# Performance work log

Hardware: AMD Instinct MI355X
Metric: run time of the kernel (lower is better)

The kernel has to match this reference:

```python
import jax, jax.numpy as jnp
import numpy as np

H = 256       # hidden_dim
E = H // 2    # operator embedding dim
T = 12        # num_tempers
O = 3         # num_ops per temper
HOPS = 4      # max_path_hops
B = 128       # batch
D = 2048      # input_dim
NCLS = 10     # task_head classes


def setup_inputs() -> dict:
    key = jax.random.key(0)
    ks = jax.random.split(key, 12)
    x = jax.random.normal(ks[0], (B, D), jnp.float32)
    N = B * (D // H)  # 1024 patch tokens
    # per-hop routed temper per patch; value == T means halt
    sampled_tempers = jax.random.randint(ks[1], (HOPS, N), 0, T + 1, jnp.int32)
    sampled_ops = jax.random.randint(ks[2], (HOPS, N), 0, O, jnp.int32)
    s1 = 1.0 / np.sqrt(H + E)
    W1 = jax.random.uniform(ks[3], (T, O, H + E, H), jnp.float32, -s1, s1)
    b1 = jax.random.uniform(ks[4], (T, O, H), jnp.float32, -s1, s1)
    s2 = 1.0 / np.sqrt(H)
    W2 = jax.random.uniform(ks[5], (T, O, H, H), jnp.float32, -s2, s2)
    b2 = jax.random.uniform(ks[6], (T, O, H), jnp.float32, -s2, s2)
    op_emb = jax.random.normal(ks[7], (T, O, E), jnp.float32)
    ln_g = jnp.ones((H,), jnp.float32)
    ln_b = jnp.zeros((H,), jnp.float32)
    Wt = jax.random.uniform(ks[8], (H, NCLS), jnp.float32, -s2, s2)
    bt = jax.random.uniform(ks[9], (NCLS,), jnp.float32, -s2, s2)
    return dict(x=x, W1=W1, b1=b1, W2=W2, b2=b2, op_emb=op_emb,
                ln_g=ln_g, ln_b=ln_b, Wt=Wt, bt=bt,
                sampled_tempers=sampled_tempers, sampled_ops=sampled_ops)


def reference(x, W1, b1, W2, b2, op_emb, ln_g, ln_b, Wt, bt,
              sampled_tempers, sampled_ops):
    Bsz, Din = x.shape
    pad = (-Din) % H
    if pad > 0:
        x = jnp.pad(x, ((0, 0), (0, pad)))
    state = x.reshape(-1, H)                       # [N, H] patch states
    active = jnp.ones((state.shape[0],), bool)     # not-yet-halted mask
    for hop in range(HOPS):
        t = sampled_tempers[hop]
        o = sampled_ops[hop]
        active = active & (t != T)                 # T == halt action
        tc = jnp.clip(t, 0, T - 1)                 # safe index for halted rows
        emb = op_emb[tc, o]                        # [N, E] op embedding gather
        xa = jnp.concatenate([state, emb], axis=-1)  # [N, H+E]
        # per-token expert weight gather + batched matvec (memory-bound dispatch)
        h = jax.nn.relu(jnp.einsum('ni,nio->no', xa, W1[tc, o]) + b1[tc, o])
        y = jax.nn.relu(jnp.einsum('ni,nio->no', h, W2[tc, o]) + b2[tc, o])
        state = jnp.where(active[:, None], y, state)
    pooled = state.reshape(Bsz, -1, H).mean(axis=1)   # [B, H]
    mu = pooled.mean(axis=-1, keepdims=True)
    var = pooled.var(axis=-1, keepdims=True)
    normed = (pooled - mu) * jax.lax.rsqrt(var + 1e-5) * ln_g + ln_b
    return normed @ Wt + bt                           # [B, 10]
```

## Files before the change

kernel.cpp:

```cpp
#include <hip/hip_runtime.h>

typedef __attribute__((ext_vector_type(8))) short short8;
typedef __attribute__((ext_vector_type(4))) float floatx4;

#define NEXP   36
#define NTOK   1024
#define HOPS   4

#define OFF_STATE   0u
#define OFF_W1B     1048576u
#define OFF_W2B     5767168u
#define OFF_C1      10485760u
#define OFF_COUNTS  10522624u
#define OFF_LISTS   10523264u

__device__ __forceinline__ unsigned short f2bf(float f) {
    unsigned u = __float_as_uint(f);
    u += 0x7FFFu + ((u >> 16) & 1u);
    return (unsigned short)(u >> 16);
}

__global__ __launch_bounds__(256) void prep_kernel(
    const float* __restrict__ x, const float* __restrict__ W1,
    const float* __restrict__ b1, const float* __restrict__ W2,
    const float* __restrict__ op_emb,
    const int* __restrict__ tempers, const int* __restrict__ ops,
    float* __restrict__ state, unsigned short* __restrict__ W1b,
    unsigned short* __restrict__ W2b, float* __restrict__ c1,
    int* __restrict__ counts, int* __restrict__ lists)
{
    const int bid = blockIdx.x;
    const int t = threadIdx.x;

    if (bid < 2304) {
        const int mat = bid / 1152;
        const int id  = bid % 1152;
        const int e   = id / 32;
        const int sub = id % 32;
        const int kb  = sub / 4;
        const int jt  = sub % 4;
        const float* src = mat ? (W2 + e * 65536) : (W1 + e * 98304);
        unsigned short* dst = (mat ? W2b : W1b) + e * 65536;
        const int j  = jt * 64 + (t & 63);
        const int ks = (t >> 6) * 8;
        short8 v;
        #pragma unroll
        for (int i = 0; i < 8; i++)
            v[i] = (short)f2bf(src[(kb * 32 + ks + i) * 256 + j]);
        *(short8*)(dst + (kb * 256 + j) * 32 + ks) = v;
    } else if (bid < 2340) {
        const int e = bid - 2304;
        __shared__ float eb[128];
        if (t < 128) eb[t] = op_emb[e * 128 + t];
        __syncthreads();
        float acc = b1[e * 256 + t];
        const float* wp = W1 + e * 98304 + 256 * 256;
        #pragma unroll 4
        for (int k = 0; k < 128; k++)
            acc += eb[k] * wp[k * 256 + t];
        c1[e * 256 + t] = acc;
    } else if (bid < 2404) {
        const int cb = bid - 2340;
        const float4* xs = (const float4*)x;
        float4* ss = (float4*)state;
        #pragma unroll
        for (int p = 0; p < 4; p++) {
            int i4 = cb * 1024 + p * 256 + t;
            ss[i4] = xs[i4];
        }
    } else {
        __shared__ int lc[HOPS * NEXP];
        if (t < HOPS * NEXP) lc[t] = 0;
        __syncthreads();
        for (int q = 0; q < 4; q++) {
            int n = q * 256 + t;
            bool act = true;
            for (int hop = 0; hop < HOPS; hop++) {
                int tt = tempers[hop * NTOK + n];
                int oo = ops[hop * NTOK + n];
                act = act && (tt != 12);
                if (act) {
                    int e = tt * 3 + oo;
                    int pos = atomicAdd(&lc[hop * NEXP + e], 1);
                    lists[(hop * NEXP + e) * NTOK + pos] = n;
                }
            }
        }
        __syncthreads();
        if (t < HOPS * NEXP) counts[t] = lc[t];
    }
}

__global__ __launch_bounds__(256) void hop_kernel(
    float* __restrict__ state,
    const unsigned short* __restrict__ W1b,
    const unsigned short* __restrict__ W2b,
    const float* __restrict__ c1, const float* __restrict__ b2,
    const int* __restrict__ counts, const int* __restrict__ lists, int hop)
{
    const int e    = blockIdx.x % NEXP;
    const int tile = blockIdx.x / NEXP;
    const int n_e  = counts[hop * NEXP + e];
    const int m0   = tile * 16;
    if (m0 >= n_e) return;
    const int mact = min(16, n_e - m0);

    __shared__ int toks[16];
    __shared__ unsigned short Ab[4096];
    __shared__ unsigned short Hb[4096];

    const int t = threadIdx.x;
    if (t < 16) toks[t] = (t < mact) ? lists[(hop * NEXP + e) * NTOK + m0 + t] : 0;
    __syncthreads();

    #pragma unroll
    for (int p = 0; p < 4; p++) {
        int idx = p * 256 + t;
        int m = idx >> 6;
        int c4 = idx & 63;
        int k = c4 * 4;
        float4 v = make_float4(0.f, 0.f, 0.f, 0.f);
        if (m < mact) v = *(const float4*)(state + toks[m] * 256 + k);
        int kb = k >> 5, g = (k >> 3) & 3, i = k & 7;
        unsigned short* d = Ab + kb * 512 + (g * 16 + m) * 8 + i;
        d[0] = f2bf(v.x); d[1] = f2bf(v.y); d[2] = f2bf(v.z); d[3] = f2bf(v.w);
    }
    __syncthreads();

    const int l = t & 63, w = t >> 6;
    const int col = l & 15, g = l >> 4;

    floatx4 acc[4];
    #pragma unroll
    for (int jt = 0; jt < 4; jt++) {
        float cv = c1[e * 256 + w * 64 + jt * 16 + col];
        acc[jt] = (floatx4){cv, cv, cv, cv};
    }
    const unsigned short* Wp = W1b + e * 65536;
    #pragma unroll
    for (int kb = 0; kb < 8; kb++) {
        short8 a = *(const short8*)(Ab + kb * 512 + l * 8);
        #pragma unroll
        for (int jt = 0; jt < 4; jt++) {
            int j = w * 64 + jt * 16 + col;
            short8 bfrg = *(const short8*)(Wp + (kb * 256 + j) * 32 + g * 8);
            acc[jt] = __builtin_amdgcn_mfma_f32_16x16x32_bf16(a, bfrg, acc[jt], 0, 0, 0);
        }
    }
    #pragma unroll
    for (int jt = 0; jt < 4; jt++) {
        int kh = w * 64 + jt * 16 + col;
        int kb2 = kh >> 5, g2 = (kh >> 3) & 3, i2 = kh & 7;
        #pragma unroll
        for (int r = 0; r < 4; r++) {
            int m = g * 4 + r;
            float vv = acc[jt][r];
            vv = vv > 0.f ? vv : 0.f;
            Hb[kb2 * 512 + (g2 * 16 + m) * 8 + i2] = f2bf(vv);
        }
    }
    __syncthreads();

    #pragma unroll
    for (int jt = 0; jt < 4; jt++) {
        float bv = b2[e * 256 + w * 64 + jt * 16 + col];
        acc[jt] = (floatx4){bv, bv, bv, bv};
    }
    const unsigned short* Wp2 = W2b + e * 65536;
    #pragma unroll
    for (int kb = 0; kb < 8; kb++) {
        short8 a = *(const short8*)(Hb + kb * 512 + l * 8);
        #pragma unroll
        for (int jt = 0; jt < 4; jt++) {
            int j = w * 64 + jt * 16 + col;
            short8 bfrg = *(const short8*)(Wp2 + (kb * 256 + j) * 32 + g * 8);
            acc[jt] = __builtin_amdgcn_mfma_f32_16x16x32_bf16(a, bfrg, acc[jt], 0, 0, 0);
        }
    }
    #pragma unroll
    for (int jt = 0; jt < 4; jt++) {
        int j = w * 64 + jt * 16 + col;
        #pragma unroll
        for (int r = 0; r < 4; r++) {
            int m = g * 4 + r;
            if (m < mact) {
                float vv = acc[jt][r];
                state[toks[m] * 256 + j] = vv > 0.f ? vv : 0.f;
            }
        }
    }
}

__global__ __launch_bounds__(256) void final_kernel(
    const float* __restrict__ state, const float* __restrict__ ln_g,
    const float* __restrict__ ln_b, const float* __restrict__ Wt,
    const float* __restrict__ bt, float* __restrict__ out)
{
    const int b = blockIdx.x, t = threadIdx.x;
    float s = 0.f;
    #pragma unroll
    for (int p = 0; p < 8; p++) s += state[(b * 8 + p) * 256 + t];
    s *= 0.125f;

    float v1 = s, v2 = s * s;
    #pragma unroll
    for (int off = 32; off; off >>= 1) {
        v1 += __shfl_down(v1, off);
        v2 += __shfl_down(v2, off);
    }
    __shared__ float red[8];
    __shared__ float stats[2];
    const int w = t >> 6, l = t & 63;
    if (l == 0) { red[w] = v1; red[4 + w] = v2; }
    __syncthreads();
    if (t == 0) {
        float su = red[0] + red[1] + red[2] + red[3];
        float sq = red[4] + red[5] + red[6] + red[7];
        float mu = su * (1.0f / 256.0f);
        float var = sq * (1.0f / 256.0f) - mu * mu;
        stats[0] = mu;
        stats[1] = rsqrtf(var + 1e-5f);
    }
    __syncthreads();
    float normed = (s - stats[0]) * stats[1] * ln_g[t] + ln_b[t];

    __shared__ float pr[40];
    #pragma unroll
    for (int c = 0; c < 10; c++) {
        float pv = normed * Wt[t * 10 + c];
        #pragma unroll
        for (int off = 32; off; off >>= 1) pv += __shfl_down(pv, off);
        if (l == 0) pr[w * 10 + c] = pv;
    }
    __syncthreads();
    if (t < 10)
        out[b * 10 + t] = pr[t] + pr[10 + t] + pr[20 + t] + pr[30 + t] + bt[t];
}

extern "C" void kernel_launch(void* const* d_in, const int* in_sizes, int n_in,
                              void* d_out, int out_size, void* d_ws, size_t ws_size,
                              hipStream_t stream)
{
    const float* x      = (const float*)d_in[0];
    const float* W1     = (const float*)d_in[1];
    const float* b1     = (const float*)d_in[2];
    const float* W2     = (const float*)d_in[3];
    const float* b2     = (const float*)d_in[4];
    const float* op_emb = (const float*)d_in[5];
    const float* ln_g   = (const float*)d_in[6];
    const float* ln_b   = (const float*)d_in[7];
    const float* Wt     = (const float*)d_in[8];
    const float* bt     = (const float*)d_in[9];
    const int* tempers  = (const int*)d_in[10];
    const int* ops      = (const int*)d_in[11];

    char* ws = (char*)d_ws;
    float* state          = (float*)(ws + OFF_STATE);
    unsigned short* W1b   = (unsigned short*)(ws + OFF_W1B);
    unsigned short* W2b   = (unsigned short*)(ws + OFF_W2B);
    float* c1             = (float*)(ws + OFF_C1);
    int* counts           = (int*)(ws + OFF_COUNTS);
    int* lists            = (int*)(ws + OFF_LISTS);
    float* out            = (float*)d_out;

    prep_kernel<<<2405, 256, 0, stream>>>(x, W1, b1, W2, op_emb, tempers, ops,
                                          state, W1b, W2b, c1, counts, lists);
    for (int hop = 0; hop < HOPS; hop++)
        hop_kernel<<<2304, 256, 0, stream>>>(state, W1b, W2b, c1, b2,
                                             counts, lists, hop);
    final_kernel<<<128, 256, 0, stream>>>(state, ln_g, ln_b, Wt, bt, out);
}
```

Measured before the change: 152.2 us.

## Fuse hop and final kernels into persistent kernel with grid barriers and job lists

Replaces the four per-hop kernel launches and the final kernel with a single persistent kernel of 256 blocks. It walks a compact job list built in prep, where each job is one (expert, 16-token tile), and separates hops with an atomic-counter grid barrier. The aim is to cut launch overhead and the mostly-empty blocks of the 2304-block grid. The barrier assumes all 256 blocks are co-resident, and it adds spin-wait cost and fewer parallel blocks per hop.

```diff
diff --git a/kernel.cpp b/kernel.cpp
--- a/kernel.cpp
+++ b/kernel.cpp
@@ -6,6 +6,7 @@
 #define NEXP   36
 #define NTOK   1024
 #define HOPS   4
+#define PGRID  256
 
 #define OFF_STATE   0u
 #define OFF_W1B     1048576u
@@ -13,6 +14,9 @@
 #define OFF_C1      10485760u
 #define OFF_COUNTS  10522624u
 #define OFF_LISTS   10523264u
+#define OFF_JOBS    11113088u
+#define OFF_NJ      11115136u
+#define OFF_BAR     11115152u
 
 __device__ __forceinline__ unsigned short f2bf(float f) {
     unsigned u = __float_as_uint(f);
@@ -27,7 +31,8 @@
     const int* __restrict__ tempers, const int* __restrict__ ops,
     float* __restrict__ state, unsigned short* __restrict__ W1b,
     unsigned short* __restrict__ W2b, float* __restrict__ c1,
-    int* __restrict__ counts, int* __restrict__ lists)
+    int* __restrict__ counts, int* __restrict__ lists,
+    int* __restrict__ jobs, int* __restrict__ njobs, int* __restrict__ bar)
 {
     const int bid = blockIdx.x;
     const int t = threadIdx.x;
@@ -71,6 +76,7 @@
     } else {
         __shared__ int lc[HOPS * NEXP];
         if (t < HOPS * NEXP) lc[t] = 0;
+        if (t == 0) bar[0] = 0;
         __syncthreads();
         for (int q = 0; q < 4; q++) {
             int n = q * 256 + t;
@@ -88,28 +94,45 @@
         }
         __syncthreads();
         if (t < HOPS * NEXP) counts[t] = lc[t];
-    }
-}
-
-__global__ __launch_bounds__(256) void hop_kernel(
-    float* __restrict__ state,
+        if (t < HOPS) {
+            int hop = t, nj = 0;
+            for (int e = 0; e < NEXP; e++) {
+                int c = lc[hop * NEXP + e];
+                for (int m0 = 0; m0 < c; m0 += 16)
+                    jobs[hop * 128 + nj++] = (m0 << 8) | e;
+            }
+            njobs[hop] = nj;
+        }
+    }
+}
+
+__device__ __forceinline__ void grid_barrier(int* bar, int target) {
+    __syncthreads();
+    if (threadIdx.x == 0) {
+        __threadfence();
+        __hip_atomic_fetch_add(bar, 1, __ATOMIC_RELEASE, __HIP_MEMORY_SCOPE_AGENT);
+        while (__hip_atomic_load(bar, __ATOMIC_ACQUIRE, __HIP_MEMORY_SCOPE_AGENT) < target)
+            __builtin_amdgcn_s_sleep(2);
+        __threadfence();
+    }
+    __syncthreads();
+}
+
+__device__ __forceinline__ void do_job(
+    int hop, int job, float* __restrict__ state,
     const unsigned short* __restrict__ W1b,
     const unsigned short* __restrict__ W2b,
     const float* __restrict__ c1, const float* __restrict__ b2,
-    const int* __restrict__ counts, const int* __restrict__ lists, int hop)
+    const int* __restrict__ counts, const int* __restrict__ lists,
+    int* toks, unsigned short* Ab, unsigned short* Hb)
 {
-    const int e    = blockIdx.x % NEXP;
-    const int tile = blockIdx.x / NEXP;
-    const int n_e  = counts[hop * NEXP + e];
-    const int m0   = tile * 16;
-    if (m0 >= n_e) return;
+    const int e   = job & 0xFF;
+    const int m0  = job >> 8;
+    const int n_e = counts[hop * NEXP + e];
     const int mact = min(16, n_e - m0);
-
-    __shared__ int toks[16];
-    __shared__ unsigned short Ab[4096];
-    __shared__ unsigned short Hb[4096];
-
     const int t = threadIdx.x;
+
+    __syncthreads();
     if (t < 16) toks[t] = (t < mact) ? lists[(hop * NEXP + e) * NTOK + m0 + t] : 0;
     __syncthreads();
 
@@ -191,12 +214,33 @@
     }
 }
 
-__global__ __launch_bounds__(256) void final_kernel(
-    const float* __restrict__ state, const float* __restrict__ ln_g,
-    const float* __restrict__ ln_b, const float* __restrict__ Wt,
-    const float* __restrict__ bt, float* __restrict__ out)
+__global__ __launch_bounds__(256) void persist_kernel(
+    float* __restrict__ state,
+    const unsigned short* __restrict__ W1b,
+    const unsigned short* __restrict__ W2b,
+    const float* __restrict__ c1, const float* __restrict__ b2,
+    const int* __restrict__ counts, const int* __restrict__ lists,
+    const int* __restrict__ jobs, const int* __restrict__ njobs,
+    int* __restrict__ bar,
+    const float* __restrict__ ln_g, const float* __restrict__ ln_b,
+    const float* __restrict__ Wt, const float* __restrict__ bt,
+    float* __restrict__ out)
 {
-    const int b = blockIdx.x, t = threadIdx.x;
+    __shared__ int toks[16];
+    __shared__ unsigned short Ab[4096];
+    __shared__ unsigned short Hb[4096];
+
+    for (int hop = 0; hop < HOPS; hop++) {
+        const int nj = njobs[hop];
+        for (int j = blockIdx.x; j < nj; j += PGRID)
+            do_job(hop, jobs[hop * 128 + j], state, W1b, W2b, c1, b2,
+                   counts, lists, toks, Ab, Hb);
+        grid_barrier(bar, (hop + 1) * PGRID);
+    }
+
+    const int b = blockIdx.x;
+    if (b >= 128) return;
+    const int t = threadIdx.x;
     float s = 0.f;
     #pragma unroll
     for (int p = 0; p < 8; p++) s += state[(b * 8 + p) * 256 + t];
@@ -261,12 +305,15 @@
     float* c1             = (float*)(ws + OFF_C1);
     int* counts           = (int*)(ws + OFF_COUNTS);
     int* lists            = (int*)(ws + OFF_LISTS);
+    int* jobs             = (int*)(ws + OFF_JOBS);
+    int* njobs            = (int*)(ws + OFF_NJ);
+    int* bar              = (int*)(ws + OFF_BAR);
     float* out            = (float*)d_out;
 
     prep_kernel<<<2405, 256, 0, stream>>>(x, W1, b1, W2, op_emb, tempers, ops,
-                                          state, W1b, W2b, c1, counts, lists);
-    for (int hop = 0; hop < HOPS; hop++)
-        hop_kernel<<<2304, 256, 0, stream>>>(state, W1b, W2b, c1, b2,
-                                             counts, lists, hop);
-    final_kernel<<<128, 256, 0, stream>>>(state, ln_g, ln_b, Wt, bt, out);
-}
+                                          state, W1b, W2b, c1, counts, lists,
+                                          jobs, njobs, bar);
+    persist_kernel<<<PGRID, 256, 0, stream>>>(state, W1b, W2b, c1, b2,
+                                              counts, lists, jobs, njobs, bar,
+                                              ln_g, ln_b, Wt, bt, out);
+}
```

Measured after the change: 319.2 us. 110% more time.

## Build compact per-hop job list and use 1024-thread blocks per expert tile

Applied to the files above, without the earlier changes.

The prep kernel now builds a dense list of (expert, tile) jobs per hop, so the hop kernel launches only 128 blocks that index into that list. Before, it launched 2304 blocks, most of which exited immediately. Each block now uses 16 waves, one per 16-column slice, instead of 4 waves each covering 64 columns. This cuts empty-block launch overhead and spreads the weight loads over more waves. In exchange, each wave has less independent MFMA work to hide latency, and the job list is built serially by 4 threads, which adds work to prep.

```diff
diff --git a/kernel.cpp b/kernel.cpp
--- a/kernel.cpp
+++ b/kernel.cpp
@@ -13,6 +13,8 @@
 #define OFF_C1      10485760u
 #define OFF_COUNTS  10522624u
 #define OFF_LISTS   10523264u
+#define OFF_JOBS    11113088u
+#define OFF_NJ      11115136u
 
 __device__ __forceinline__ unsigned short f2bf(float f) {
     unsigned u = __float_as_uint(f);
@@ -27,7 +29,8 @@
     const int* __restrict__ tempers, const int* __restrict__ ops,
     float* __restrict__ state, unsigned short* __restrict__ W1b,
     unsigned short* __restrict__ W2b, float* __restrict__ c1,
-    int* __restrict__ counts, int* __restrict__ lists)
+    int* __restrict__ counts, int* __restrict__ lists,
+    int* __restrict__ jobs, int* __restrict__ njobs)
 {
     const int bid = blockIdx.x;
     const int t = threadIdx.x;
@@ -88,21 +91,31 @@
         }
         __syncthreads();
         if (t < HOPS * NEXP) counts[t] = lc[t];
-    }
-}
-
-__global__ __launch_bounds__(256) void hop_kernel(
+        if (t < HOPS) {
+            int hop = t, nj = 0;
+            for (int e = 0; e < NEXP; e++) {
+                int c = lc[hop * NEXP + e];
+                for (int m0 = 0; m0 < c; m0 += 16)
+                    jobs[hop * 128 + nj++] = (m0 << 8) | e;
+            }
+            njobs[hop] = nj;
+        }
+    }
+}
+
+__global__ __launch_bounds__(1024) void hop_kernel(
     float* __restrict__ state,
     const unsigned short* __restrict__ W1b,
     const unsigned short* __restrict__ W2b,
     const float* __restrict__ c1, const float* __restrict__ b2,
-    const int* __restrict__ counts, const int* __restrict__ lists, int hop)
-{
-    const int e    = blockIdx.x % NEXP;
-    const int tile = blockIdx.x / NEXP;
-    const int n_e  = counts[hop * NEXP + e];
-    const int m0   = tile * 16;
-    if (m0 >= n_e) return;
+    const int* __restrict__ counts, const int* __restrict__ lists,
+    const int* __restrict__ jobs, const int* __restrict__ njobs, int hop)
+{
+    if (blockIdx.x >= njobs[hop]) return;
+    const int job = jobs[hop * 128 + blockIdx.x];
+    const int e   = job & 0xFF;
+    const int m0  = job >> 8;
+    const int n_e = counts[hop * NEXP + e];
     const int mact = min(16, n_e - m0);
 
     __shared__ int toks[16];
@@ -113,12 +126,9 @@
     if (t < 16) toks[t] = (t < mact) ? lists[(hop * NEXP + e) * NTOK + m0 + t] : 0;
     __syncthreads();
 
-    #pragma unroll
-    for (int p = 0; p < 4; p++) {
-        int idx = p * 256 + t;
-        int m = idx >> 6;
-        int c4 = idx & 63;
-        int k = c4 * 4;
+    {
+        int m = t >> 6;
+        int k = (t & 63) * 4;
         float4 v = make_float4(0.f, 0.f, 0.f, 0.f);
         if (m < mact) v = *(const float4*)(state + toks[m] * 256 + k);
         int kb = k >> 5, g = (k >> 3) & 3, i = k & 7;
@@ -129,64 +139,50 @@
 
     const int l = t & 63, w = t >> 6;
     const int col = l & 15, g = l >> 4;
-
-    floatx4 acc[4];
-    #pragma unroll
-    for (int jt = 0; jt < 4; jt++) {
-        float cv = c1[e * 256 + w * 64 + jt * 16 + col];
-        acc[jt] = (floatx4){cv, cv, cv, cv};
+    const int j = w * 16 + col;
+
+    floatx4 acc;
+    {
+        float cv = c1[e * 256 + j];
+        acc = (floatx4){cv, cv, cv, cv};
     }
     const unsigned short* Wp = W1b + e * 65536;
     #pragma unroll
     for (int kb = 0; kb < 8; kb++) {
         short8 a = *(const short8*)(Ab + kb * 512 + l * 8);
-        #pragma unroll
-        for (int jt = 0; jt < 4; jt++) {
-            int j = w * 64 + jt * 16 + col;
-            short8 bfrg = *(const short8*)(Wp + (kb * 256 + j) * 32 + g * 8);
-            acc[jt] = __builtin_amdgcn_mfma_f32_16x16x32_bf16(a, bfrg, acc[jt], 0, 0, 0);
-        }
-    }
-    #pragma unroll
-    for (int jt = 0; jt < 4; jt++) {
-        int kh = w * 64 + jt * 16 + col;
+        short8 bfrg = *(const short8*)(Wp + (kb * 256 + j) * 32 + g * 8);
+        acc = __builtin_amdgcn_mfma_f32_16x16x32_bf16(a, bfrg, acc, 0, 0, 0);
+    }
+    {
+        int kh = j;
         int kb2 = kh >> 5, g2 = (kh >> 3) & 3, i2 = kh & 7;
         #pragma unroll
         for (int r = 0; r < 4; r++) {
             int m = g * 4 + r;
-            float vv = acc[jt][r];
+            float vv = acc[r];
             vv = vv > 0.f ? vv : 0.f;
             Hb[kb2 * 512 + (g2 * 16 + m) * 8 + i2] = f2bf(vv);
         }
     }
     __syncthreads();
 
-    #pragma unroll
-    for (int jt = 0; jt < 4; jt++) {
-        float bv = b2[e * 256 + w * 64 + jt * 16 + col];
-        acc[jt] = (floatx4){bv, bv, bv, bv};
+    {
+        float bv = b2[e * 256 + j];
+        acc = (floatx4){bv, bv, bv, bv};
     }
     const unsigned short* Wp2 = W2b + e * 65536;
     #pragma unroll
     for (int kb = 0; kb < 8; kb++) {
         short8 a = *(const short8*)(Hb + kb * 512 + l * 8);
-        #pragma unroll
-        for (int jt = 0; jt < 4; jt++) {
-            int j = w * 64 + jt * 16 + col;
-            short8 bfrg = *(const short8*)(Wp2 + (kb * 256 + j) * 32 + g * 8);
-            acc[jt] = __builtin_amdgcn_mfma_f32_16x16x32_bf16(a, bfrg, acc[jt], 0, 0, 0);
-        }
-    }
-    #pragma unroll
-    for (int jt = 0; jt < 4; jt++) {
-        int j = w * 64 + jt * 16 + col;
-        #pragma unroll
-        for (int r = 0; r < 4; r++) {
-            int m = g * 4 + r;
-            if (m < mact) {
-                float vv = acc[jt][r];
-                state[toks[m] * 256 + j] = vv > 0.f ? vv : 0.f;
-            }
+        short8 bfrg = *(const short8*)(Wp2 + (kb * 256 + j) * 32 + g * 8);
+        acc = __builtin_amdgcn_mfma_f32_16x16x32_bf16(a, bfrg, acc, 0, 0, 0);
+    }
+    #pragma unroll
+    for (int r = 0; r < 4; r++) {
+        int m = g * 4 + r;
+        if (m < mact) {
+            float vv = acc[r];
+            state[toks[m] * 256 + j] = vv > 0.f ? vv : 0.f;
         }
     }
 }
@@ -261,12 +257,15 @@
     float* c1             = (float*)(ws + OFF_C1);
     int* counts           = (int*)(ws + OFF_COUNTS);
     int* lists            = (int*)(ws + OFF_LISTS);
+    int* jobs             = (int*)(ws + OFF_JOBS);
+    int* njobs            = (int*)(ws + OFF_NJ);
     float* out            = (float*)d_out;
 
     prep_kernel<<<2405, 256, 0, stream>>>(x, W1, b1, W2, op_emb, tempers, ops,
-                                          state, W1b, W2b, c1, counts, lists);
+                                          state, W1b, W2b, c1, counts, lists,
+                                          jobs, njobs);
     for (int hop = 0; hop < HOPS; hop++)
-        hop_kernel<<<2304, 256, 0, stream>>>(state, W1b, W2b, c1, b2,
-                                             counts, lists, hop);
+        hop_kernel<<<128, 1024, 0, stream>>>(state, W1b, W2b, c1, b2,
+                                             counts, lists, jobs, njobs, hop);
     final_kernel<<<128, 256, 0, stream>>>(state, ln_g, ln_b, Wt, bt, out);
 }
```

Result: faster. 142.4 us (-6.4%).
